# Kernel optimization log

Hardware: AMD Instinct MI355X
Metric: run time of the kernel (lower is better)

Reference implementation:

```python
import jax, jax.numpy as jnp
import numpy as np

N = 200000          # nodes
E = 6400000         # edges (before self-loops)
L = 4               # layer_n
H = 9               # hidden_channels (hardcoded in module)
G = 2000            # graphs in batch
C = 2               # num_classes
NEG_SLOPE = 0.2     # GATConv default leaky_relu slope for attention logits


def setup_inputs() -> dict:
    key = jax.random.key(0)
    ks = jax.random.split(key, 9)
    x = jax.random.normal(ks[0], (N, H), dtype=jnp.float32)
    edge_index = jax.random.randint(ks[1], (2, E), 0, N, dtype=jnp.int32)
    batch = jnp.sort(jax.random.randint(ks[2], (N,), 0, G, dtype=jnp.int32))
    W = jax.random.normal(ks[3], (L, H, H), dtype=jnp.float32) * 0.3
    att_src = jax.random.normal(ks[4], (L, H), dtype=jnp.float32) * 0.3
    att_dst = jax.random.normal(ks[5], (L, H), dtype=jnp.float32) * 0.3
    bias = jax.random.normal(ks[6], (L, H), dtype=jnp.float32) * 0.1
    fc_w = jax.random.normal(ks[7], (L * H, C), dtype=jnp.float32) * 0.2
    fc_b = jax.random.normal(ks[8], (C,), dtype=jnp.float32) * 0.1
    return dict(x=x, edge_index=edge_index, batch=batch, W=W,
                att_src=att_src, att_dst=att_dst, bias=bias,
                fc_w=fc_w, fc_b=fc_b)


def _gat_layer(x, W_l, a_src, a_dst, b_l, src, dst, n):
    # h: [N, H] transformed features (linear, no bias per PyG default)
    h = x @ W_l
    alpha_s = h @ a_src            # [N]
    alpha_d = h @ a_dst            # [N]
    # attention logits per edge (src -> dst), GAT softmax grouped by dst
    e = jax.nn.leaky_relu(alpha_s[src] + alpha_d[dst], NEG_SLOPE)  # [E']
    e = e - jax.ops.segment_max(e, dst, num_segments=n)[dst]
    w = jnp.exp(e)
    denom = jax.ops.segment_sum(w, dst, num_segments=n)[dst]
    alpha = w / denom              # [E']
    out = jax.ops.segment_sum(alpha[:, None] * h[src], dst, num_segments=n)
    return out + b_l


def reference(x, edge_index, batch, W, att_src, att_dst, bias, fc_w, fc_b):
    n = x.shape[0]
    loops = jnp.arange(n, dtype=edge_index.dtype)
    src = jnp.concatenate([edge_index[0], loops])  # add_self_loops=True
    dst = jnp.concatenate([edge_index[1], loops])
    jk = []
    h = x
    for l in range(L):
        h = _gat_layer(h, W[l], att_src[l], att_dst[l], bias[l], src, dst, n)
        h = jax.nn.relu(h)
        jk.append(h)
    jk = jnp.concatenate(jk, axis=1)               # [N, L*H]
    pooled = jax.ops.segment_max(jk, batch, num_segments=G)
    pooled = jnp.where(jnp.isfinite(pooled), pooled, 0.0)  # guard empty graphs
    # dropout is identity at inference
    return pooled @ fc_w + fc_b
```

## Files before the change

kernel.cpp:

```cpp
#include <hip/hip_runtime.h>
#include <hip/hip_fp16.h>

#define Nn 200000
#define Ee 6400000
#define EP 6600000
#define Hh 9
#define Ll 4
#define Gg 2000
#define Cc 2
#define JK 36
#define NCB ((Nn + 1023) >> 10)
#define EPB 8192
#define NBLKA ((EP + EPB - 1) / EPB)
#define NB ((Nn + 255) / 256)
#define NPB 32
#define NAB (Nn / NPB)
#define CAP 3072
#define CAPB 36864
#define HTS (NCB + 1)

union H2F { __half2 h; float f; };


__global__ __launch_bounds__(256) void kA_scatter(
    const int* __restrict__ src, const int* __restrict__ dst,
    int* __restrict__ ctot, int* __restrict__ histT,
    unsigned* __restrict__ bucketed)
{
    __shared__ unsigned pbuf[EPB];
    __shared__ int lh[NCB];
    __shared__ int s[256];
    int t = threadIdx.x;
    if (t < NCB) lh[t] = 0;
    __syncthreads();
    const int base = blockIdx.x * EPB;
    const int nseg = min(EPB, EP - base);
    for (int j = t; j < nseg; j += 256) {
        int e = base + j;
        int d = (e < Ee) ? dst[e] : (e - Ee);
        atomicAdd(&lh[d >> 10], 1);
    }
    __syncthreads();
    int v = (t < NCB) ? lh[t] : 0;
    s[t] = v; __syncthreads();
    for (int off = 1; off < 256; off <<= 1) {
        int u = (t >= off) ? s[t - off] : 0;
        __syncthreads();
        s[t] += u;
        __syncthreads();
    }
    int* hrow = histT + (size_t)blockIdx.x * HTS;
    if (t < NCB) {
        int ex = s[t] - v;
        lh[t] = ex;
        hrow[t] = ex;
        if (v) atomicAdd(&ctot[t], v);
    }
    if (t == 0) hrow[NCB] = nseg;
    __syncthreads();
    for (int j = t; j < nseg; j += 256) {
        int e = base + j;
        int sv, d;
        if (e < Ee) { sv = src[e]; d = dst[e]; } else { sv = e - Ee; d = sv; }
        int pos = atomicAdd(&lh[d >> 10], 1);
        pbuf[pos] = (unsigned)sv | ((unsigned)(d & 1023) << 18);
    }
    __syncthreads();
    for (int j = t; j < nseg; j += 256)
        bucketed[base + j] = pbuf[j];
}

__global__ __launch_bounds__(256) void k_scan(
    const int* __restrict__ ctot, int* __restrict__ cbase,
    int* __restrict__ row_ptr)
{
    __shared__ int s[256];
    int t = threadIdx.x;
    int v = (t < NCB) ? ctot[t] : 0;
    s[t] = v; __syncthreads();
    for (int off = 1; off < 256; off <<= 1) {
        int u = (t >= off) ? s[t - off] : 0;
        __syncthreads();
        s[t] += u;
        __syncthreads();
    }
    if (t < NCB) cbase[t] = s[t] - v;
    if (t == 0) { cbase[NCB] = EP; row_ptr[Nn] = EP; }
}

__global__ __launch_bounds__(1024) void kB_csr(
    const unsigned* __restrict__ bucketed, const int* __restrict__ histT,
    const int* __restrict__ cbase, int* __restrict__ row_ptr,
    int* __restrict__ csr_src)
{
    __shared__ int bh[1024];
    __shared__ int cur[1024];
    __shared__ unsigned pbuf[CAPB];
    const int k = blockIdx.x;
    const int t = threadIdx.x;
    const int w = t >> 6, lane = t & 63;
    bh[t] = 0;
    __syncthreads();
    const int base_k = cbase[k];
    const int nseg_b = cbase[k + 1] - base_k;
    const bool fit = (nseg_b <= CAPB);
    for (int b = w; b < NBLKA; b += 16) {
        const int* hrow = histT + (size_t)b * HTS;
        int s0 = hrow[k], s1 = hrow[k + 1];
        int rb = b * EPB;
        for (int j = s0 + lane; j < s1; j += 64)
            atomicAdd(&bh[(__builtin_nontemporal_load(bucketed + rb + j) >> 18) & 1023], 1);
    }
    __syncthreads();
    int v = bh[t];
    for (int off = 1; off < 1024; off <<= 1) {
        int u = (t >= off) ? bh[t - off] : 0;
        __syncthreads();
        bh[t] += u;
        __syncthreads();
    }
    int ex = bh[t] - v;
    int node = (k << 10) + t;
    if (node < Nn) row_ptr[node] = base_k + ex;
    cur[t] = ex;
    __syncthreads();
    if (fit) {
        for (int b = w; b < NBLKA; b += 16) {
            const int* hrow = histT + (size_t)b * HTS;
            int s0 = hrow[k], s1 = hrow[k + 1];
            int rb = b * EPB;
            for (int j = s0 + lane; j < s1; j += 64) {
                unsigned p = __builtin_nontemporal_load(bucketed + rb + j);
                int pos = atomicAdd(&cur[(p >> 18) & 1023], 1);
                pbuf[pos] = p & 0x3FFFFu;
            }
        }
        __syncthreads();
        for (int j = t; j < nseg_b; j += 1024)
            csr_src[base_k + j] = (int)pbuf[j];
    } else {
        for (int b = w; b < NBLKA; b += 16) {
            const int* hrow = histT + (size_t)b * HTS;
            int s0 = hrow[k], s1 = hrow[k + 1];
            int rb = b * EPB;
            for (int j = s0 + lane; j < s1; j += 64) {
                unsigned p = bucketed[rb + j];
                int pos = base_k + atomicAdd(&cur[(p >> 18) & 1023], 1);
                csr_src[pos] = (int)(p & 0x3FFFFu);
            }
        }
    }
}


__global__ __launch_bounds__(256) void k_transform(
    const float* __restrict__ xin, int xstride,
    const float* __restrict__ Wl,
    const float* __restrict__ adst,
    float4* __restrict__ A, __half* __restrict__ Bh, float* __restrict__ D)
{
    int i = blockIdx.x * blockDim.x + threadIdx.x;
    if (i >= Nn) return;
    const float* xp = xin + (size_t)i * xstride;
    float xi[Hh];
#pragma unroll
    for (int k = 0; k < Hh; ++k) xi[k] = xp[k];
    float hv[Hh];
#pragma unroll
    for (int j = 0; j < Hh; ++j) {
        float s = 0.f;
#pragma unroll
        for (int k = 0; k < Hh; ++k) s += xi[k] * Wl[k * Hh + j];
        hv[j] = s;
    }
    float ad = 0.f;
#pragma unroll
    for (int j = 0; j < Hh; ++j) ad += hv[j] * adst[j];
    H2F u01, u23, u45, u67;
    u01.h = __floats2half2_rn(hv[0], hv[1]);
    u23.h = __floats2half2_rn(hv[2], hv[3]);
    u45.h = __floats2half2_rn(hv[4], hv[5]);
    u67.h = __floats2half2_rn(hv[6], hv[7]);
    A[i] = make_float4(u01.f, u23.f, u45.f, u67.f);
    Bh[i] = __float2half(hv[8]);
    D[i] = ad;
}

__global__ __launch_bounds__(256) void k_node_agg(
    const int* __restrict__ rp, const int* __restrict__ csr,
    const float4* __restrict__ A, const __half* __restrict__ Bh,
    const float* __restrict__ D, const float* __restrict__ asrc,
    const float* __restrict__ biasl,
    float* __restrict__ jk, int l)
{
    __shared__ int scsr[CAP];
    __shared__ int srp[NPB + 1];
    const int nbase = blockIdx.x * NPB;
    const int t = threadIdx.x;
    if (t <= NPB) srp[t] = rp[nbase + t];
    __syncthreads();
    const int beg_blk = srp[0];
    const int nseg = srp[NPB] - beg_blk;
    const bool use_lds = (nseg <= CAP);
    if (use_lds)
        for (int j = t; j < nseg; j += 256)
            scsr[j] = __builtin_nontemporal_load(csr + beg_blk + j);
    __syncthreads();

    const float s0 = asrc[0], s1 = asrc[1], s2 = asrc[2], s3 = asrc[3],
                s4 = asrc[4], s5 = asrc[5], s6 = asrc[6], s7 = asrc[7],
                s8 = asrc[8];

    const int ni = t >> 3;
    const int q  = t & 7;
    const int i  = nbase + ni;
    const float c = D[i];
    float a0=0,a1=0,a2=0,a3=0,a4=0,a5=0,a6=0,a7=0,a8=0,den=0;
    if (use_lds) {
        int idx = srp[ni] - beg_blk + q;
        const int iend = srp[ni + 1] - beg_blk;
        int s = (idx < iend) ? scsr[idx] : 0;
        float4 F = A[s];
        __half hb = Bh[s];
        while (idx < iend) {
            int nidx = idx + 8;
            int sn = (nidx < iend) ? scsr[nidx] : 0;
            float4 Fn = A[sn];
            __half hbn = Bh[sn];
            H2F u; float2 p;
            u.f = F.x; p = __half22float2(u.h); float x0 = p.x, x1 = p.y;
            u.f = F.y; p = __half22float2(u.h); float x2 = p.x, x3 = p.y;
            u.f = F.z; p = __half22float2(u.h); float x4 = p.x, x5 = p.y;
            u.f = F.w; p = __half22float2(u.h); float x6 = p.x, x7 = p.y;
            float x8 = __half2float(hb);
            float as = x0*s0 + x1*s1 + x2*s2 + x3*s3 + x4*s4
                     + x5*s5 + x6*s6 + x7*s7 + x8*s8;
            float lg = as + c;
            lg = lg > 0.f ? lg : 0.2f * lg;
            float w = __expf(lg);
            a0 += w*x0; a1 += w*x1; a2 += w*x2; a3 += w*x3; a4 += w*x4;
            a5 += w*x5; a6 += w*x6; a7 += w*x7; a8 += w*x8;
            den += w;
            F = Fn; hb = hbn; idx = nidx;
        }
    } else {
        for (int e = srp[ni] + q; e < srp[ni + 1]; e += 8) {
            int s = csr[e];
            float4 F = A[s];
            __half hb = Bh[s];
            H2F u; float2 p;
            u.f = F.x; p = __half22float2(u.h); float x0 = p.x, x1 = p.y;
            u.f = F.y; p = __half22float2(u.h); float x2 = p.x, x3 = p.y;
            u.f = F.z; p = __half22float2(u.h); float x4 = p.x, x5 = p.y;
            u.f = F.w; p = __half22float2(u.h); float x6 = p.x, x7 = p.y;
            float x8 = __half2float(hb);
            float as = x0*s0 + x1*s1 + x2*s2 + x3*s3 + x4*s4
                     + x5*s5 + x6*s6 + x7*s7 + x8*s8;
            float lg = as + c;
            lg = lg > 0.f ? lg : 0.2f * lg;
            float w = __expf(lg);
            a0 += w*x0; a1 += w*x1; a2 += w*x2; a3 += w*x3; a4 += w*x4;
            a5 += w*x5; a6 += w*x6; a7 += w*x7; a8 += w*x8;
            den += w;
        }
    }
#pragma unroll
    for (int m = 1; m <= 4; m <<= 1) {
        a0 += __shfl_xor(a0, m); a1 += __shfl_xor(a1, m);
        a2 += __shfl_xor(a2, m); a3 += __shfl_xor(a3, m);
        a4 += __shfl_xor(a4, m); a5 += __shfl_xor(a5, m);
        a6 += __shfl_xor(a6, m); a7 += __shfl_xor(a7, m);
        a8 += __shfl_xor(a8, m); den += __shfl_xor(den, m);
    }
    if (q == 0) {
        float inv = 1.f / den;
        float* jp = jk + (size_t)i * JK + l * Hh;
        float o;
        o = fmaxf(a0*inv + biasl[0], 0.f); __builtin_nontemporal_store(o, jp + 0);
        o = fmaxf(a1*inv + biasl[1], 0.f); __builtin_nontemporal_store(o, jp + 1);
        o = fmaxf(a2*inv + biasl[2], 0.f); __builtin_nontemporal_store(o, jp + 2);
        o = fmaxf(a3*inv + biasl[3], 0.f); __builtin_nontemporal_store(o, jp + 3);
        o = fmaxf(a4*inv + biasl[4], 0.f); __builtin_nontemporal_store(o, jp + 4);
        o = fmaxf(a5*inv + biasl[5], 0.f); __builtin_nontemporal_store(o, jp + 5);
        o = fmaxf(a6*inv + biasl[6], 0.f); __builtin_nontemporal_store(o, jp + 6);
        o = fmaxf(a7*inv + biasl[7], 0.f); __builtin_nontemporal_store(o, jp + 7);
        o = fmaxf(a8*inv + biasl[8], 0.f); __builtin_nontemporal_store(o, jp + 8);
    }
}


__global__ __launch_bounds__(256) void k_graph_ptr(
    const int* __restrict__ batch, int* __restrict__ gp)
{
    int i = blockIdx.x * 256 + threadIdx.x;
    if (i >= Nn) return;
    int b = batch[i];
    if (i == 0) {
        for (int g = 0; g <= b; ++g) gp[g] = 0;
    } else {
        int pb = batch[i - 1];
        for (int g = pb + 1; g <= b; ++g) gp[g] = i;
    }
    if (i == Nn - 1) {
        for (int g = b + 1; g <= Gg; ++g) gp[g] = Nn;
    }
}

__global__ __launch_bounds__(256) void k_pool_seg(
    const float* __restrict__ jk, const int* __restrict__ gp,
    float* __restrict__ pooled)
{
    int t = blockIdx.x * 256 + threadIdx.x;
    if (t >= Gg * JK) return;
    int g = t / JK, col = t - g * JK;
    int beg = gp[g], end = gp[g + 1];
    float m = 0.f;
    for (int i = beg; i < end; ++i)
        m = fmaxf(m, jk[(size_t)i * JK + col]);
    pooled[t] = m;
}

__global__ __launch_bounds__(256) void k_fc(
    const float* __restrict__ pooled, const float* __restrict__ fcw,
    const float* __restrict__ fcb, float* __restrict__ out)
{
    int t = blockIdx.x * blockDim.x + threadIdx.x;
    if (t >= Gg * Cc) return;
    int g = t / Cc, c = t - g * Cc;
    float s = fcb[c];
    const float* pp = pooled + (size_t)g * JK;
#pragma unroll
    for (int j = 0; j < JK; ++j) s += pp[j] * fcw[j * Cc + c];
    out[t] = s;
}

extern "C" void kernel_launch(void* const* d_in, const int* in_sizes, int n_in,
                              void* d_out, int out_size, void* d_ws, size_t ws_size,
                              hipStream_t stream) {
    const float* x      = (const float*)d_in[0];
    const int*   ei     = (const int*)d_in[1];
    const int*   batch  = (const int*)d_in[2];
    const float* W      = (const float*)d_in[3];
    const float* a_src  = (const float*)d_in[4];
    const float* a_dst  = (const float*)d_in[5];
    const float* bias   = (const float*)d_in[6];
    const float* fc_w   = (const float*)d_in[7];
    const float* fc_b   = (const float*)d_in[8];
    float* out = (float*)d_out;

    float* ws        = (float*)d_ws;
    float4* A        = (float4*)ws;
    __half* Bh       = (__half*)(ws + (size_t)Nn * 4);
    float* D         = (float*)((char*)Bh + (size_t)Nn * sizeof(__half));
    float* jk        = D + Nn;
    float* pooled    = jk + (size_t)Nn * JK;
    int* row_ptr     = (int*)(pooled + (size_t)Gg * JK);
    int* gp          = row_ptr + Nn + 1;
    int* ctot        = gp + Gg + 1;
    int* cbase       = ctot + NCB;
    int* csr_src     = cbase + NCB + 1;
    int* histT       = (int*)ws;
    unsigned* bucketed = (unsigned*)jk;

    const int* srcp = ei;
    const int* dstp = ei + Ee;

    hipMemsetAsync(ctot, 0, NCB * sizeof(int), stream);
    kA_scatter<<<NBLKA, 256, 0, stream>>>(srcp, dstp, ctot, histT, bucketed);
    k_scan    <<<1, 256, 0, stream>>>(ctot, cbase, row_ptr);
    kB_csr    <<<NCB, 1024, 0, stream>>>(bucketed, histT, cbase, row_ptr, csr_src);

    for (int l = 0; l < Ll; ++l) {
        const float* xin = (l == 0) ? x : (jk + (size_t)(l - 1) * Hh);
        int xstride      = (l == 0) ? Hh : JK;
        k_transform<<<NB, 256, 0, stream>>>(xin, xstride, W + l * Hh * Hh,
                                            a_dst + l * Hh, A, Bh, D);
        k_node_agg<<<NAB, 256, 0, stream>>>(row_ptr, csr_src, A, Bh, D,
                                            a_src + l * Hh, bias + l * Hh, jk, l);
    }
    k_graph_ptr<<<NB, 256, 0, stream>>>(batch, gp);
    k_pool_seg<<<(Gg * JK + 255) / 256, 256, 0, stream>>>(jk, gp, pooled);
    k_fc<<<(Gg * Cc + 255) / 256, 256, 0, stream>>>(pooled, fc_w, fc_b, out);
}
```

Baseline: 599.8 us.

## Compute per-node degrees with global atomics in scatter, drop CSR histogram pass

```diff
diff --git a/kernel.cpp b/kernel.cpp
--- a/kernel.cpp
+++ b/kernel.cpp
@@ -24,7 +24,7 @@
 
 __global__ __launch_bounds__(256) void kA_scatter(
     const int* __restrict__ src, const int* __restrict__ dst,
-    int* __restrict__ ctot, int* __restrict__ histT,
+    int* __restrict__ deg, int* __restrict__ histT,
     unsigned* __restrict__ bucketed)
 {
     __shared__ unsigned pbuf[EPB];
@@ -39,6 +39,7 @@
         int e = base + j;
         int d = (e < Ee) ? dst[e] : (e - Ee);
         atomicAdd(&lh[d >> 10], 1);
+        atomicAdd(&deg[d], 1);
     }
     __syncthreads();
     int v = (t < NCB) ? lh[t] : 0;
@@ -54,7 +55,6 @@
         int ex = s[t] - v;
         lh[t] = ex;
         hrow[t] = ex;
-        if (v) atomicAdd(&ctot[t], v);
     }
     if (t == 0) hrow[NCB] = nseg;
     __syncthreads();
@@ -70,6 +70,26 @@
         bucketed[base + j] = pbuf[j];
 }
 
+__global__ __launch_bounds__(1024) void k_scan_part(
+    const int* __restrict__ deg, int* __restrict__ row_ptr,
+    int* __restrict__ ctot)
+{
+    __shared__ int bh[1024];
+    const int k = blockIdx.x;
+    const int t = threadIdx.x;
+    const int node = (k << 10) + t;
+    int v = (node < Nn) ? deg[node] : 0;
+    bh[t] = v; __syncthreads();
+    for (int off = 1; off < 1024; off <<= 1) {
+        int u = (t >= off) ? bh[t - off] : 0;
+        __syncthreads();
+        bh[t] += u;
+        __syncthreads();
+    }
+    if (node < Nn) row_ptr[node] = bh[t] - v;
+    if (t == 1023) ctot[k] = bh[1023];
+}
+
 __global__ __launch_bounds__(256) void k_scan(
     const int* __restrict__ ctot, int* __restrict__ cbase,
     int* __restrict__ row_ptr)
@@ -93,46 +113,57 @@
     const int* __restrict__ cbase, int* __restrict__ row_ptr,
     int* __restrict__ csr_src)
 {
-    __shared__ int bh[1024];
+    __shared__ int2 hb[NBLKA];
     __shared__ int cur[1024];
     __shared__ unsigned pbuf[CAPB];
     const int k = blockIdx.x;
     const int t = threadIdx.x;
     const int w = t >> 6, lane = t & 63;
-    bh[t] = 0;
-    __syncthreads();
+    for (int j = t; j < NBLKA; j += 1024) {
+        const int* hrow = histT + (size_t)j * HTS + k;
+        hb[j] = make_int2(hrow[0], hrow[1]);
+    }
     const int base_k = cbase[k];
     const int nseg_b = cbase[k + 1] - base_k;
     const bool fit = (nseg_b <= CAPB);
-    for (int b = w; b < NBLKA; b += 16) {
-        const int* hrow = histT + (size_t)b * HTS;
-        int s0 = hrow[k], s1 = hrow[k + 1];
-        int rb = b * EPB;
-        for (int j = s0 + lane; j < s1; j += 64)
-            atomicAdd(&bh[(__builtin_nontemporal_load(bucketed + rb + j) >> 18) & 1023], 1);
-    }
-    __syncthreads();
-    int v = bh[t];
-    for (int off = 1; off < 1024; off <<= 1) {
-        int u = (t >= off) ? bh[t - off] : 0;
-        __syncthreads();
-        bh[t] += u;
-        __syncthreads();
-    }
-    int ex = bh[t] - v;
-    int node = (k << 10) + t;
-    if (node < Nn) row_ptr[node] = base_k + ex;
-    cur[t] = ex;
+    const int node = (k << 10) + t;
+    if (node < Nn) {
+        int rel = row_ptr[node];
+        row_ptr[node] = base_k + rel;
+        cur[t] = rel;
+    } else {
+        cur[t] = 0;
+    }
     __syncthreads();
     if (fit) {
-        for (int b = w; b < NBLKA; b += 16) {
-            const int* hrow = histT + (size_t)b * HTS;
-            int s0 = hrow[k], s1 = hrow[k + 1];
-            int rb = b * EPB;
-            for (int j = s0 + lane; j < s1; j += 64) {
-                unsigned p = __builtin_nontemporal_load(bucketed + rb + j);
-                int pos = atomicAdd(&cur[(p >> 18) & 1023], 1);
-                pbuf[pos] = p & 0x3FFFFu;
+        for (int b = w; b < NBLKA; b += 16 * 4) {
+            int2 es[4]; unsigned ps[4];
+#pragma unroll
+            for (int u = 0; u < 4; ++u) {
+                int bb = b + 16 * u;
+                int2 e = (bb < NBLKA) ? hb[bb] : make_int2(0, 0);
+                es[u] = e;
+                int j = e.x + lane;
+                ps[u] = (j < e.y)
+                    ? __builtin_nontemporal_load(bucketed + (size_t)bb * EPB + j)
+                    : 0u;
+            }
+#pragma unroll
+            for (int u = 0; u < 4; ++u) {
+                int bb = b + 16 * u;
+                if (bb >= NBLKA) break;
+                int j = es[u].x + lane;
+                if (j < es[u].y) {
+                    unsigned p = ps[u];
+                    int pos = atomicAdd(&cur[(p >> 18) & 1023], 1);
+                    pbuf[pos] = p & 0x3FFFFu;
+                }
+                for (j += 64; j < es[u].y; j += 64) {
+                    unsigned p = __builtin_nontemporal_load(
+                        bucketed + (size_t)bb * EPB + j);
+                    int pos = atomicAdd(&cur[(p >> 18) & 1023], 1);
+                    pbuf[pos] = p & 0x3FFFFu;
+                }
             }
         }
         __syncthreads();
@@ -140,10 +171,9 @@
             csr_src[base_k + j] = (int)pbuf[j];
     } else {
         for (int b = w; b < NBLKA; b += 16) {
-            const int* hrow = histT + (size_t)b * HTS;
-            int s0 = hrow[k], s1 = hrow[k + 1];
+            int2 e = hb[b];
             int rb = b * EPB;
-            for (int j = s0 + lane; j < s1; j += 64) {
+            for (int j = e.x + lane; j < e.y; j += 64) {
                 unsigned p = bucketed[rb + j];
                 int pos = base_k + atomicAdd(&cur[(p >> 18) & 1023], 1);
                 csr_src[pos] = (int)(p & 0x3FFFFu);
@@ -360,15 +390,17 @@
     int* cbase       = ctot + NCB;
     int* csr_src     = cbase + NCB + 1;
     int* histT       = (int*)ws;
+    int* deg         = (int*)((char*)ws + (1 << 20));
     unsigned* bucketed = (unsigned*)jk;
 
     const int* srcp = ei;
     const int* dstp = ei + Ee;
 
-    hipMemsetAsync(ctot, 0, NCB * sizeof(int), stream);
-    kA_scatter<<<NBLKA, 256, 0, stream>>>(srcp, dstp, ctot, histT, bucketed);
-    k_scan    <<<1, 256, 0, stream>>>(ctot, cbase, row_ptr);
-    kB_csr    <<<NCB, 1024, 0, stream>>>(bucketed, histT, cbase, row_ptr, csr_src);
+    hipMemsetAsync(deg, 0, Nn * sizeof(int), stream);
+    kA_scatter <<<NBLKA, 256, 0, stream>>>(srcp, dstp, deg, histT, bucketed);
+    k_scan_part<<<NCB, 1024, 0, stream>>>(deg, row_ptr, ctot);
+    k_scan     <<<1, 256, 0, stream>>>(ctot, cbase, row_ptr);
+    kB_csr     <<<NCB, 1024, 0, stream>>>(bucketed, histT, cbase, row_ptr, csr_src);
 
     for (int l = 0; l < Ll; ++l) {
         const float* xin = (l == 0) ? x : (jk + (size_t)(l - 1) * Hh);
```

After: 735.5 us. 1.23x slower.
